# Kernel tuning notes

Hardware: AMD Instinct MI355X
Metric: run time of the kernel (lower is better)

The kernel has to match this reference:

```python
import jax, jax.numpy as jnp
import numpy as np

HEADS = 16
D_MODEL = 1024
GROUP = 4
SEQ = 2048
HEAD_DIM = D_MODEL // HEADS          # 64
KV_HEADS = HEADS // GROUP            # 4


def rope_tables(head_dim, seq_len, base=10000.0):
    # NOTE: faithful to source: exp = -2*arange(0,d,2)/d  (steps of 2 -> base^{-4j/d})
    exp = -2.0 * jnp.arange(0, head_dim, 2, dtype=jnp.float32) / head_dim
    thetas = jnp.power(base, exp)                       # [d/2]
    m = jnp.arange(seq_len, dtype=jnp.float32)          # [S]
    freq = jnp.outer(m, thetas)                         # [S, d/2]
    return jnp.cos(freq), jnp.sin(freq)


def apply_rope(x, cos, sin):
    # x: [B,S,H,D]; complex rotation on consecutive pairs
    B, S, H, D = x.shape
    xr = x.reshape(B, S, H, D // 2, 2)
    x0, x1 = xr[..., 0], xr[..., 1]
    c = cos[None, :S, None, :]
    s = sin[None, :S, None, :]
    out = jnp.stack([x0 * c - x1 * s, x0 * s + x1 * c], axis=-1)
    return out.reshape(B, S, H, D)


def setup_inputs() -> dict:
    key = jax.random.key(0)
    ks = jax.random.split(key, 8)
    B = 1
    q = jax.random.normal(ks[0], (B, SEQ, D_MODEL), dtype=jnp.float32)
    k = jax.random.normal(ks[1], (B, SEQ, D_MODEL), dtype=jnp.float32)
    v = jax.random.normal(ks[2], (B, SEQ, D_MODEL), dtype=jnp.float32)
    mask = jnp.tril(jnp.ones((SEQ, SEQ), dtype=jnp.int32))[None]  # causal [B,S,S]
    sc = 0.02
    Wq = jax.random.normal(ks[3], (D_MODEL, D_MODEL), dtype=jnp.float32) * sc
    Wk = jax.random.normal(ks[4], (D_MODEL, D_MODEL // GROUP), dtype=jnp.float32) * sc
    Wv = jax.random.normal(ks[5], (D_MODEL, D_MODEL // GROUP), dtype=jnp.float32) * sc
    Wo = jax.random.normal(ks[6], (D_MODEL, D_MODEL), dtype=jnp.float32) * sc
    bq = jnp.zeros((D_MODEL,), jnp.float32)
    bk = jnp.zeros((D_MODEL // GROUP,), jnp.float32)
    bv = jnp.zeros((D_MODEL // GROUP,), jnp.float32)
    bo = jnp.zeros((D_MODEL,), jnp.float32)
    return {"q": q, "k": k, "v": v, "mask": mask, "Wq": Wq, "bq": bq,
            "Wk": Wk, "bk": bk, "Wv": Wv, "bv": bv, "Wo": Wo, "bo": bo}


def reference(q, k, v, mask, Wq, bq, Wk, bk, Wv, bv, Wo, bo):
    B, S, _ = q.shape
    cos, sin = rope_tables(HEAD_DIM, S)
    qh = (q @ Wq + bq).reshape(B, S, HEADS, HEAD_DIM)
    kh = (k @ Wk + bk).reshape(B, S, KV_HEADS, HEAD_DIM)
    vh = (v @ Wv + bv).reshape(B, S, KV_HEADS, HEAD_DIM)
    qh = apply_rope(qh, cos, sin)
    kh = apply_rope(kh, cos, sin)
    qh = qh.transpose(0, 2, 1, 3)                       # [B,H,S,D]
    kh = kh.transpose(0, 2, 1, 3)                       # [B,Hkv,S,D]
    vh = vh.transpose(0, 2, 1, 3)
    # torch .repeat tiles: query head j attends kv head j % KV_HEADS
    kh = jnp.tile(kh, (1, GROUP, 1, 1))                 # [B,H,S,D]
    vh = jnp.tile(vh, (1, GROUP, 1, 1))
    scores = jnp.einsum('bhqd,bhkd->bhqk', qh, kh) / jnp.sqrt(
        jnp.asarray(HEAD_DIM, dtype=qh.dtype))
    scores = jnp.where(mask[:, None, :, :] == 0, -jnp.inf, scores)
    attn = jax.nn.softmax(scores, axis=-1)
    out = jnp.einsum('bhqk,bhkd->bhqd', attn, vh)
    out = out.transpose(0, 2, 1, 3).reshape(B, S, D_MODEL)
    return out @ Wo + bo
```

## Files before the change

### kernel.cpp

```cpp
#include <hip/hip_runtime.h>
#include <hip/hip_bf16.h>
#include <math.h>


#define SEQ 2048
#define DM 1024
#define HD 64

using u16 = unsigned short;
typedef __attribute__((ext_vector_type(8))) short bf16x8;
typedef __attribute__((ext_vector_type(4))) float f32x4;

#define QSCALE 0.18033688011112042f

__device__ __forceinline__ u16 f2b(float f) {
    union { float f; unsigned int i; } v; v.f = f;
    unsigned int u = v.i;
    return (u16)((u + 0x7fffu + ((u >> 16) & 1u)) >> 16);
}
__device__ __forceinline__ u16 f2b_fast(float f) {
    union { float f; unsigned int i; } v; v.f = f;
    return (u16)((v.i + 0x8000u) >> 16);
}

__global__ __launch_bounds__(256) void prep_kernel(
    const float* __restrict__ qin, const float* __restrict__ kin, const float* __restrict__ vin,
    const float* __restrict__ Wq, const float* __restrict__ Wk,
    const float* __restrict__ Wv, const float* __restrict__ Wo,
    u16* __restrict__ Xq, u16* __restrict__ Xk, u16* __restrict__ Xv,
    u16* __restrict__ Wt, u16* __restrict__ wot, float2* __restrict__ rope)
{
    const int b = blockIdx.x;
    const int t = threadIdx.x;

    if (b < 640) {
        __shared__ short T[64][72];
        const float* W; u16* dst; int N, t0, rowoff;
        if (b < 256)      { W = Wq; dst = Wt;  N = 1024; t0 = b;       rowoff = 0; }
        else if (b < 320) { W = Wk; dst = Wt;  N = 256;  t0 = b - 256; rowoff = 1024; }
        else if (b < 384) { W = Wv; dst = Wt;  N = 256;  t0 = b - 320; rowoff = 1280; }
        else              { W = Wo; dst = wot; N = 1024; t0 = b - 384; rowoff = 0; }
        const int ntn = N >> 6;
        const int k0 = (t0 / ntn) * 64, n0 = (t0 % ntn) * 64;
        const int r = t >> 4, c4 = (t & 15) * 4;
        #pragma unroll
        for (int rr = 0; rr < 4; ++rr) {
            const int k = r + rr * 16;
            float4 w4 = *reinterpret_cast<const float4*>(W + (size_t)(k0 + k) * N + n0 + c4);
            T[c4 + 0][k] = (short)f2b(w4.x);
            T[c4 + 1][k] = (short)f2b(w4.y);
            T[c4 + 2][k] = (short)f2b(w4.z);
            T[c4 + 3][k] = (short)f2b(w4.w);
        }
        __syncthreads();
        const int n = t >> 2, ck = (t & 3) * 16;
        if (b < 384) {
            const int nt = (rowoff + n0) >> 6, kt = k0 >> 6;
            char* dp = (char*)(dst + (size_t)(nt * 16 + kt) * 4096) + n * 128;
            const int g0 = (t & 3) * 2, rx = n & 7;
            *reinterpret_cast<bf16x8*>(dp + (((g0    ) ^ rx) << 4)) =
                *reinterpret_cast<const bf16x8*>(&T[n][ck]);
            *reinterpret_cast<bf16x8*>(dp + (((g0 + 1) ^ rx) << 4)) =
                *reinterpret_cast<const bf16x8*>(&T[n][ck + 8]);
        } else {
            u16* dp = dst + (size_t)(n0 + n) * DM + k0 + ck;
            *reinterpret_cast<bf16x8*>(dp)     = *reinterpret_cast<const bf16x8*>(&T[n][ck]);
            *reinterpret_cast<bf16x8*>(dp + 8) = *reinterpret_cast<const bf16x8*>(&T[n][ck + 8]);
        }
    } else if (b < 1408) {
        const int idx = b - 640;
        const int which = idx >> 8;
        const int ib = idx & 255;
        const float* src = (which == 0) ? qin : (which == 1) ? kin : vin;
        u16* dst = (which == 0) ? Xq : (which == 1) ? Xk : Xv;
        const int m  = ib * 8 + (t >> 5);
        const int mt = m >> 6, r = m & 63, rx = r & 7;
        const int col0 = (t & 31) * 32;
        const float* sp = src + (size_t)m * 1024 + col0;
        #pragma unroll
        for (int c = 0; c < 4; ++c) {
            float4 x0 = *reinterpret_cast<const float4*>(sp + c * 8);
            float4 x1 = *reinterpret_cast<const float4*>(sp + c * 8 + 4);
            bf16x8 o;
            o[0] = (short)f2b(x0.x); o[1] = (short)f2b(x0.y);
            o[2] = (short)f2b(x0.z); o[3] = (short)f2b(x0.w);
            o[4] = (short)f2b(x1.x); o[5] = (short)f2b(x1.y);
            o[6] = (short)f2b(x1.z); o[7] = (short)f2b(x1.w);
            const int col = col0 + c * 8;
            const int kt = col >> 6, g = (col & 63) >> 3;
            char* dp = (char*)(dst + (size_t)(mt * 16 + kt) * 4096)
                     + r * 128 + ((g ^ rx) << 4);
            *reinterpret_cast<bf16x8*>(dp) = o;
        }
    } else {
        const int m = (b - 1408) * 256 + t;
        float2* rp = rope + (size_t)m * 32;
        for (int pi = 0; pi < 32; ++pi) {
            const float theta = exp2f(-0.8304820237f * (float)pi);
            float sn, cs;
            sincosf((float)m * theta, &sn, &cs);
            rp[pi] = make_float2(cs, sn);
        }
    }
}

__global__ __launch_bounds__(256) void proj_mfma(
    const u16* __restrict__ Xq, const u16* __restrict__ Xk, const u16* __restrict__ Xv,
    const u16* __restrict__ Wt,
    const float* __restrict__ bq, const float* __restrict__ bk, const float* __restrict__ bv,
    const float2* __restrict__ rope,
    u16* __restrict__ Qr, u16* __restrict__ Kr, u16* __restrict__ Vrt)
{
    const int n0 = blockIdx.x * 64, m0 = blockIdx.y * 64;
    const int zone = (n0 < 1024) ? 0 : (n0 < 1280) ? 1 : 2;
    const u16* __restrict__ Az = (zone == 0) ? Xq : (zone == 1) ? Xk : Xv;

    __shared__ __align__(16) u16 As[2][4096];
    __shared__ __align__(16) u16 Bs[2][4096];

    const int t = threadIdx.x;
    const int w = t >> 6, lane = t & 63, lm = lane & 15, quad = lane >> 4;

    f32x4 acc[4] = { {0,0,0,0}, {0,0,0,0}, {0,0,0,0}, {0,0,0,0} };

    const char* Ag = (const char*)(Az + (size_t)(m0 >> 6) * 16 * 4096);
    const char* Bg = (const char*)(Wt + (size_t)(n0 >> 6) * 16 * 4096);

    auto stage = [&](int bufi, int kti) {
        const char* gA = Ag + (size_t)kti * 8192 + w * 2048 + lane * 16;
        const char* gB = Bg + (size_t)kti * 8192 + w * 2048 + lane * 16;
        char* lA = (char*)&As[bufi][0] + w * 2048;
        char* lB = (char*)&Bs[bufi][0] + w * 2048;
        #pragma unroll
        for (int i = 0; i < 2; ++i) {
            __builtin_amdgcn_global_load_lds(
                (const __attribute__((address_space(1))) unsigned int*)(gA + i * 1024),
                (__attribute__((address_space(3))) unsigned int*)(lA + i * 1024), 16, 0, 0);
            __builtin_amdgcn_global_load_lds(
                (const __attribute__((address_space(1))) unsigned int*)(gB + i * 1024),
                (__attribute__((address_space(3))) unsigned int*)(lB + i * 1024), 16, 0, 0);
        }
    };

    stage(0, 0);
    __syncthreads();

    const int rA = 16 * w + lm;
    const int axr = rA & 7;
    for (int kt = 0; kt < 16; ++kt) {
        const int buf = kt & 1;
        if (kt < 15) stage(buf ^ 1, kt + 1);
        const char* Ab = (const char*)&As[buf][0];
        const char* Bb = (const char*)&Bs[buf][0];
        bf16x8 af0 = *reinterpret_cast<const bf16x8*>(Ab + rA * 128 + (((quad    ) ^ axr) << 4));
        bf16x8 af1 = *reinterpret_cast<const bf16x8*>(Ab + rA * 128 + (((4 | quad) ^ axr) << 4));
        #pragma unroll
        for (int nb = 0; nb < 4; ++nb) {
            const int rB = 16 * nb + lm, bxr = rB & 7;
            bf16x8 b0 = *reinterpret_cast<const bf16x8*>(Bb + rB * 128 + (((quad    ) ^ bxr) << 4));
            bf16x8 b1 = *reinterpret_cast<const bf16x8*>(Bb + rB * 128 + (((4 | quad) ^ bxr) << 4));
            acc[nb] = __builtin_amdgcn_mfma_f32_16x16x32_bf16(af0, b0, acc[nb], 0, 0, 0);
            acc[nb] = __builtin_amdgcn_mfma_f32_16x16x32_bf16(af1, b1, acc[nb], 0, 0, 0);
        }
        __syncthreads();
    }

    const float* __restrict__ bias = (zone == 0) ? bq : (zone == 1) ? bk : bv;
    const int nbase = (zone == 0) ? n0 : (zone == 1) ? (n0 - 1024) : (n0 - 1280);
    const int head = nbase >> 6;
    #pragma unroll
    for (int nb = 0; nb < 4; ++nb) {
        const int d = 16 * nb + lm;
        const float bvv = bias[nbase + d];
        float vals[4];
        #pragma unroll
        for (int r = 0; r < 4; ++r) vals[r] = acc[nb][r] + bvv;
        if (zone != 2) {
            const int pi = d >> 1;
            const bool odd = (lm & 1);
            const float sca = (zone == 0) ? QSCALE : 1.0f;
            u16* op = (zone == 0 ? Qr : Kr) + (size_t)head * SEQ * HD;
            #pragma unroll
            for (int r = 0; r < 4; ++r) {
                const int m = m0 + 16 * w + quad * 4 + r;
                const float2 cs2 = rope[(size_t)m * 32 + pi];
                float x  = vals[r];
                float xp = __shfl_xor(x, 1);
                float o  = (odd ? (xp * cs2.y + x * cs2.x)
                                : (x * cs2.x - xp * cs2.y)) * sca;
                op[(size_t)m * HD + d] = f2b(o);
            }
        } else {
            u16* vp = Vrt + ((size_t)head * HD + d) * SEQ;
            #pragma unroll
            for (int r = 0; r < 4; ++r) {
                const int m = m0 + 16 * w + quad * 4 + r;
                const int within = m & 63;
                const int pos = (m & ~63) + 4 * (within & 15) + (within >> 4);
                vp[pos] = f2b(vals[r]);
            }
        }
    }
}

__global__ __launch_bounds__(256) void attn_mfma(
    const u16* __restrict__ Qr, const u16* __restrict__ Kr, const u16* __restrict__ Vrt,
    u16* __restrict__ AO)
{
    const int bid = blockIdx.x;
    const int h  = bid & 15;
    const int qt = (bid < 256) ? (bid >> 4) : 31 - ((bid - 256) >> 4);
    const int kvh = h & 3;

    __shared__ u16 Ks[2][64][72];
    __shared__ u16 Vt[2][64][72];
    __shared__ u16 Ps[4][16][76];

    const int t = threadIdx.x;
    const int w = t >> 6, lane = t & 63, lm = lane & 15, quad = lane >> 4;

    {
        const int row = lane >> 2, c = (lane & 3) * 16;
        const u16* qp = Qr + ((size_t)h * SEQ + qt * 64 + w * 16 + row) * HD + c;
        *reinterpret_cast<bf16x8*>(&Ps[w][row][c])     = *reinterpret_cast<const bf16x8*>(qp);
        *reinterpret_cast<bf16x8*>(&Ps[w][row][c + 8]) = *reinterpret_cast<const bf16x8*>(qp + 8);
    }
    const bf16x8 aq0 = *reinterpret_cast<const bf16x8*>(&Ps[w][lm][quad * 8]);
    const bf16x8 aq1 = *reinterpret_cast<const bf16x8*>(&Ps[w][lm][32 + quad * 8]);

    f32x4 O[4] = { {0,0,0,0}, {0,0,0,0}, {0,0,0,0}, {0,0,0,0} };
    float lp[4] = { 0.f, 0.f, 0.f, 0.f };

    const int srow = t >> 2, sc2 = (t & 3) * 16;
    const u16* kb_ = Kr  + ((size_t)kvh * SEQ + srow) * HD + sc2;
    const u16* vb_ = Vrt + ((size_t)kvh * HD + srow) * SEQ + sc2;
    bf16x8 kR0 = *reinterpret_cast<const bf16x8*>(kb_);
    bf16x8 kR1 = *reinterpret_cast<const bf16x8*>(kb_ + 8);
    bf16x8 vR0 = *reinterpret_cast<const bf16x8*>(vb_);
    bf16x8 vR1 = *reinterpret_cast<const bf16x8*>(vb_ + 8);

    for (int kt = 0; kt <= qt; ++kt) {
        const int buf = kt & 1;
        *reinterpret_cast<bf16x8*>(&Ks[buf][srow][sc2])     = kR0;
        *reinterpret_cast<bf16x8*>(&Ks[buf][srow][sc2 + 8]) = kR1;
        *reinterpret_cast<bf16x8*>(&Vt[buf][srow][sc2])     = vR0;
        *reinterpret_cast<bf16x8*>(&Vt[buf][srow][sc2 + 8]) = vR1;
        if (kt < qt) {
            kR0 = *reinterpret_cast<const bf16x8*>(kb_ + (size_t)(kt + 1) * 64 * HD);
            kR1 = *reinterpret_cast<const bf16x8*>(kb_ + (size_t)(kt + 1) * 64 * HD + 8);
            vR0 = *reinterpret_cast<const bf16x8*>(vb_ + (size_t)(kt + 1) * 64);
            vR1 = *reinterpret_cast<const bf16x8*>(vb_ + (size_t)(kt + 1) * 64 + 8);
        }
        __syncthreads();

        f32x4 s[4];
        #pragma unroll
        for (int nb = 0; nb < 4; ++nb) {
            bf16x8 b0 = *reinterpret_cast<const bf16x8*>(&Ks[buf][16 * nb + lm][quad * 8]);
            bf16x8 b1 = *reinterpret_cast<const bf16x8*>(&Ks[buf][16 * nb + lm][32 + quad * 8]);
            f32x4 zz = { 0.f, 0.f, 0.f, 0.f };
            zz = __builtin_amdgcn_mfma_f32_16x16x32_bf16(aq0, b0, zz, 0, 0, 0);
            s[nb] = __builtin_amdgcn_mfma_f32_16x16x32_bf16(aq1, b1, zz, 0, 0, 0);
        }

        if (kt == qt) {
            #pragma unroll
            for (int nb = 0; nb < 4; ++nb)
                #pragma unroll
                for (int r = 0; r < 4; ++r)
                    if (16 * nb + lm > 16 * w + quad * 4 + r) s[nb][r] = -INFINITY;
        }

        #pragma unroll
        for (int r = 0; r < 4; ++r) {
            u16 pk[4];
            #pragma unroll
            for (int nb = 0; nb < 4; ++nb) {
                float e = __builtin_amdgcn_exp2f(fminf(s[nb][r], 126.f));
                lp[r] += e;
                pk[nb] = f2b_fast(e);
            }
            *reinterpret_cast<uint2*>(&Ps[w][quad * 4 + r][4 * lm]) =
                *reinterpret_cast<uint2*>(pk);
        }

        const bf16x8 ap0 = *reinterpret_cast<const bf16x8*>(&Ps[w][lm][quad * 8]);
        const bf16x8 ap1 = *reinterpret_cast<const bf16x8*>(&Ps[w][lm][32 + quad * 8]);
        #pragma unroll
        for (int db = 0; db < 4; ++db) {
            bf16x8 v0 = *reinterpret_cast<const bf16x8*>(&Vt[buf][16 * db + lm][quad * 8]);
            bf16x8 v1 = *reinterpret_cast<const bf16x8*>(&Vt[buf][16 * db + lm][32 + quad * 8]);
            O[db] = __builtin_amdgcn_mfma_f32_16x16x32_bf16(ap0, v0, O[db], 0, 0, 0);
            O[db] = __builtin_amdgcn_mfma_f32_16x16x32_bf16(ap1, v1, O[db], 0, 0, 0);
        }
    }

    #pragma unroll
    for (int r = 0; r < 4; ++r) {
        #pragma unroll
        for (int off = 1; off < 16; off <<= 1)
            lp[r] += __shfl_xor(lp[r], off);
        const float inv = 1.0f / lp[r];
        const size_t row = (size_t)(qt * 64 + 16 * w + quad * 4 + r) * DM + (size_t)h * HD;
        #pragma unroll
        for (int db = 0; db < 4; ++db)
            AO[row + 16 * db + lm] = f2b(O[db][r] * inv);
    }
}

__global__ __launch_bounds__(256) void oproj_mfma(
    const u16* __restrict__ AO, const u16* __restrict__ wot,
    const float* __restrict__ bo, float* __restrict__ out)
{
    __shared__ short As[2][64][72];
    __shared__ short Bs[2][64][72];
    const int t = threadIdx.x;
    const int w = t >> 6, lane = t & 63, lm = lane & 15, quad = lane >> 4;
    const int m0 = blockIdx.y * 64, n0 = blockIdx.x * 64;
    const int sr = t >> 2, sc = (t & 3) * 16;

    f32x4 acc[4] = { {0,0,0,0}, {0,0,0,0}, {0,0,0,0}, {0,0,0,0} };

    const u16* ap_ = AO  + (size_t)(m0 + sr) * DM + sc;
    const u16* bp_ = wot + (size_t)(n0 + sr) * DM + sc;
    bf16x8 aR0 = *reinterpret_cast<const bf16x8*>(ap_);
    bf16x8 aR1 = *reinterpret_cast<const bf16x8*>(ap_ + 8);
    bf16x8 bR0 = *reinterpret_cast<const bf16x8*>(bp_);
    bf16x8 bR1 = *reinterpret_cast<const bf16x8*>(bp_ + 8);

    for (int k0 = 0; k0 < DM; k0 += 64) {
        const int buf = (k0 >> 6) & 1;
        *reinterpret_cast<bf16x8*>(&As[buf][sr][sc])     = aR0;
        *reinterpret_cast<bf16x8*>(&As[buf][sr][sc + 8]) = aR1;
        *reinterpret_cast<bf16x8*>(&Bs[buf][sr][sc])     = bR0;
        *reinterpret_cast<bf16x8*>(&Bs[buf][sr][sc + 8]) = bR1;
        if (k0 + 64 < DM) {
            aR0 = *reinterpret_cast<const bf16x8*>(ap_ + k0 + 64);
            aR1 = *reinterpret_cast<const bf16x8*>(ap_ + k0 + 72);
            bR0 = *reinterpret_cast<const bf16x8*>(bp_ + k0 + 64);
            bR1 = *reinterpret_cast<const bf16x8*>(bp_ + k0 + 72);
        }
        __syncthreads();
        bf16x8 af0 = *reinterpret_cast<const bf16x8*>(&As[buf][16 * w + lm][quad * 8]);
        bf16x8 af1 = *reinterpret_cast<const bf16x8*>(&As[buf][16 * w + lm][32 + quad * 8]);
        #pragma unroll
        for (int nb = 0; nb < 4; ++nb) {
            bf16x8 b0 = *reinterpret_cast<const bf16x8*>(&Bs[buf][16 * nb + lm][quad * 8]);
            bf16x8 b1 = *reinterpret_cast<const bf16x8*>(&Bs[buf][16 * nb + lm][32 + quad * 8]);
            acc[nb] = __builtin_amdgcn_mfma_f32_16x16x32_bf16(af0, b0, acc[nb], 0, 0, 0);
            acc[nb] = __builtin_amdgcn_mfma_f32_16x16x32_bf16(af1, b1, acc[nb], 0, 0, 0);
        }
        __syncthreads();
    }

    #pragma unroll
    for (int nb = 0; nb < 4; ++nb) {
        const int dl = 16 * nb + lm;
        const float bv = bo[n0 + dl];
        #pragma unroll
        for (int r = 0; r < 4; ++r) {
            const int m = m0 + 16 * w + quad * 4 + r;
            out[(size_t)m * DM + n0 + dl] = acc[nb][r] + bv;
        }
    }
}

extern "C" void kernel_launch(void* const* d_in, const int* in_sizes, int n_in,
                              void* d_out, int out_size, void* d_ws, size_t ws_size,
                              hipStream_t stream)
{
    const float* q  = (const float*)d_in[0];
    const float* k  = (const float*)d_in[1];
    const float* v  = (const float*)d_in[2];
    const float* Wq = (const float*)d_in[4];
    const float* bq = (const float*)d_in[5];
    const float* Wk = (const float*)d_in[6];
    const float* bk = (const float*)d_in[7];
    const float* Wv = (const float*)d_in[8];
    const float* bv = (const float*)d_in[9];
    const float* Wo = (const float*)d_in[10];
    const float* bo = (const float*)d_in[11];
    float* out = (float*)d_out;

    u16* Xq  = (u16*)d_ws;
    u16* Xk  = Xq  + (size_t)SEQ * DM;
    u16* Xv  = Xk  + (size_t)SEQ * DM;
    u16* Wt  = Xv  + (size_t)SEQ * DM;
    u16* wot = Wt  + (size_t)1536 * 1024;
    u16* Qr  = wot + (size_t)1024 * 1024;
    u16* Kr  = Qr  + (size_t)16 * SEQ * HD;
    u16* Vrt = Kr  + (size_t)4 * SEQ * HD;
    u16* AO  = Vrt + (size_t)4 * SEQ * HD;
    float2* rope = (float2*)(AO + (size_t)SEQ * DM);

    hipLaunchKernelGGL(prep_kernel, dim3(1416), dim3(256), 0, stream,
                       q, k, v, Wq, Wk, Wv, Wo, Xq, Xk, Xv, Wt, wot, rope);
    hipLaunchKernelGGL(proj_mfma, dim3(24, 32), dim3(256), 0, stream,
                       Xq, Xk, Xv, Wt, bq, bk, bv, rope, Qr, Kr, Vrt);
    hipLaunchKernelGGL(attn_mfma, dim3(512), dim3(256), 0, stream,
                       Qr, Kr, Vrt, AO);
    hipLaunchKernelGGL(oproj_mfma, dim3(16, 32), dim3(256), 0, stream,
                       AO, wot, bo, out);
}
```

Baseline: 165.4 us.

## Halve attention query tile to 32 rows with XOR-swizzled unpadded LDS

The attention kernel now uses 128-thread blocks covering 32 query rows each, launched as 1024 blocks. This doubles the grid for better CU fill and causal load balance, but each K/V tile is now loaded by twice as many blocks. K/V shared tiles drop their padding and use an XOR swizzle on 16-byte chunks to avoid bank conflicts. The bf16 conversion of softmax probabilities now uses the packed v_cvt_pk_bf16_f32 instruction instead of manual bit rounding.

```diff
diff --git a/kernel.cpp b/kernel.cpp
--- a/kernel.cpp
+++ b/kernel.cpp
@@ -18,9 +18,10 @@
     unsigned int u = v.i;
     return (u16)((u + 0x7fffu + ((u >> 16) & 1u)) >> 16);
 }
-__device__ __forceinline__ u16 f2b_fast(float f) {
-    union { float f; unsigned int i; } v; v.f = f;
-    return (u16)((v.i + 0x8000u) >> 16);
+__device__ __forceinline__ unsigned int cvtpk(float lo, float hi) {
+    unsigned int r;
+    asm("v_cvt_pk_bf16_f32 %0, %1, %2" : "=v"(r) : "v"(lo), "v"(hi));
+    return r;
 }
 
 __global__ __launch_bounds__(256) void prep_kernel(
@@ -203,25 +204,25 @@
     }
 }
 
-__global__ __launch_bounds__(256) void attn_mfma(
+__global__ __launch_bounds__(128) void attn_mfma(
     const u16* __restrict__ Qr, const u16* __restrict__ Kr, const u16* __restrict__ Vrt,
     u16* __restrict__ AO)
 {
     const int bid = blockIdx.x;
     const int h  = bid & 15;
-    const int qt = (bid < 256) ? (bid >> 4) : 31 - ((bid - 256) >> 4);
+    const int qt = (bid < 512) ? (bid >> 4) : 63 - ((bid - 512) >> 4);
     const int kvh = h & 3;
 
-    __shared__ u16 Ks[2][64][72];
-    __shared__ u16 Vt[2][64][72];
-    __shared__ u16 Ps[4][16][76];
+    __shared__ __align__(16) u16 Ks[2][64][64];
+    __shared__ __align__(16) u16 Vt[2][64][64];
+    __shared__ u16 Ps[2][16][76];
 
     const int t = threadIdx.x;
     const int w = t >> 6, lane = t & 63, lm = lane & 15, quad = lane >> 4;
 
     {
         const int row = lane >> 2, c = (lane & 3) * 16;
-        const u16* qp = Qr + ((size_t)h * SEQ + qt * 64 + w * 16 + row) * HD + c;
+        const u16* qp = Qr + ((size_t)h * SEQ + qt * 32 + w * 16 + row) * HD + c;
         *reinterpret_cast<bf16x8*>(&Ps[w][row][c])     = *reinterpret_cast<const bf16x8*>(qp);
         *reinterpret_cast<bf16x8*>(&Ps[w][row][c + 8]) = *reinterpret_cast<const bf16x8*>(qp + 8);
     }
@@ -231,65 +232,78 @@
     f32x4 O[4] = { {0,0,0,0}, {0,0,0,0}, {0,0,0,0}, {0,0,0,0} };
     float lp[4] = { 0.f, 0.f, 0.f, 0.f };
 
-    const int srow = t >> 2, sc2 = (t & 3) * 16;
-    const u16* kb_ = Kr  + ((size_t)kvh * SEQ + srow) * HD + sc2;
-    const u16* vb_ = Vrt + ((size_t)kvh * HD + srow) * SEQ + sc2;
-    bf16x8 kR0 = *reinterpret_cast<const bf16x8*>(kb_);
-    bf16x8 kR1 = *reinterpret_cast<const bf16x8*>(kb_ + 8);
-    bf16x8 vR0 = *reinterpret_cast<const bf16x8*>(vb_);
-    bf16x8 vR1 = *reinterpret_cast<const bf16x8*>(vb_ + 8);
-
-    for (int kt = 0; kt <= qt; ++kt) {
+    const int srow = t >> 1, half = t & 1, sxr = srow & 7;
+    const u16* kb_ = Kr  + ((size_t)kvh * SEQ + srow) * HD + half * 32;
+    const u16* vb_ = Vrt + ((size_t)kvh * HD + srow) * SEQ + half * 32;
+    bf16x8 kR[4], vR[4];
+    #pragma unroll
+    for (int i = 0; i < 4; ++i) {
+        kR[i] = *reinterpret_cast<const bf16x8*>(kb_ + 8 * i);
+        vR[i] = *reinterpret_cast<const bf16x8*>(vb_ + 8 * i);
+    }
+
+    const int KT = qt >> 1;
+    const int radd = 32 * (qt & 1);
+    for (int kt = 0; kt <= KT; ++kt) {
         const int buf = kt & 1;
-        *reinterpret_cast<bf16x8*>(&Ks[buf][srow][sc2])     = kR0;
-        *reinterpret_cast<bf16x8*>(&Ks[buf][srow][sc2 + 8]) = kR1;
-        *reinterpret_cast<bf16x8*>(&Vt[buf][srow][sc2])     = vR0;
-        *reinterpret_cast<bf16x8*>(&Vt[buf][srow][sc2 + 8]) = vR1;
-        if (kt < qt) {
-            kR0 = *reinterpret_cast<const bf16x8*>(kb_ + (size_t)(kt + 1) * 64 * HD);
-            kR1 = *reinterpret_cast<const bf16x8*>(kb_ + (size_t)(kt + 1) * 64 * HD + 8);
-            vR0 = *reinterpret_cast<const bf16x8*>(vb_ + (size_t)(kt + 1) * 64);
-            vR1 = *reinterpret_cast<const bf16x8*>(vb_ + (size_t)(kt + 1) * 64 + 8);
+        {
+            char* kdst = (char*)&Ks[buf][0][0] + srow * 128;
+            char* vdst = (char*)&Vt[buf][0][0] + srow * 128;
+            #pragma unroll
+            for (int i = 0; i < 4; ++i) {
+                *reinterpret_cast<bf16x8*>(kdst + (((4 * half + i) ^ sxr) << 4)) = kR[i];
+                *reinterpret_cast<bf16x8*>(vdst + (((4 * half + i) ^ sxr) << 4)) = vR[i];
+            }
+        }
+        if (kt < KT) {
+            #pragma unroll
+            for (int i = 0; i < 4; ++i) {
+                kR[i] = *reinterpret_cast<const bf16x8*>(kb_ + (size_t)(kt + 1) * 64 * HD + 8 * i);
+                vR[i] = *reinterpret_cast<const bf16x8*>(vb_ + (size_t)(kt + 1) * 64 + 8 * i);
+            }
         }
         __syncthreads();
 
+        const int xr = lm & 7;
         f32x4 s[4];
         #pragma unroll
         for (int nb = 0; nb < 4; ++nb) {
-            bf16x8 b0 = *reinterpret_cast<const bf16x8*>(&Ks[buf][16 * nb + lm][quad * 8]);
-            bf16x8 b1 = *reinterpret_cast<const bf16x8*>(&Ks[buf][16 * nb + lm][32 + quad * 8]);
+            const char* kb = (const char*)&Ks[buf][0][0] + (16 * nb + lm) * 128;
+            bf16x8 b0 = *reinterpret_cast<const bf16x8*>(kb + (((quad    ) ^ xr) << 4));
+            bf16x8 b1 = *reinterpret_cast<const bf16x8*>(kb + (((4 | quad) ^ xr) << 4));
             f32x4 zz = { 0.f, 0.f, 0.f, 0.f };
             zz = __builtin_amdgcn_mfma_f32_16x16x32_bf16(aq0, b0, zz, 0, 0, 0);
             s[nb] = __builtin_amdgcn_mfma_f32_16x16x32_bf16(aq1, b1, zz, 0, 0, 0);
         }
 
-        if (kt == qt) {
+        if (kt == KT) {
             #pragma unroll
             for (int nb = 0; nb < 4; ++nb)
                 #pragma unroll
                 for (int r = 0; r < 4; ++r)
-                    if (16 * nb + lm > 16 * w + quad * 4 + r) s[nb][r] = -INFINITY;
+                    if (16 * nb + lm > 16 * w + quad * 4 + r + radd) s[nb][r] = -INFINITY;
         }
 
         #pragma unroll
         for (int r = 0; r < 4; ++r) {
-            u16 pk[4];
-            #pragma unroll
-            for (int nb = 0; nb < 4; ++nb) {
-                float e = __builtin_amdgcn_exp2f(fminf(s[nb][r], 126.f));
-                lp[r] += e;
-                pk[nb] = f2b_fast(e);
-            }
-            *reinterpret_cast<uint2*>(&Ps[w][quad * 4 + r][4 * lm]) =
-                *reinterpret_cast<uint2*>(pk);
+            float e0 = __builtin_amdgcn_exp2f(fminf(s[0][r], 126.f));
+            float e1 = __builtin_amdgcn_exp2f(fminf(s[1][r], 126.f));
+            float e2 = __builtin_amdgcn_exp2f(fminf(s[2][r], 126.f));
+            float e3 = __builtin_amdgcn_exp2f(fminf(s[3][r], 126.f));
+            lp[r] += (e0 + e1) + (e2 + e3);
+            uint2 pk2;
+            pk2.x = cvtpk(e0, e1);
+            pk2.y = cvtpk(e2, e3);
+            *reinterpret_cast<uint2*>(&Ps[w][quad * 4 + r][4 * lm]) = pk2;
         }
 
         const bf16x8 ap0 = *reinterpret_cast<const bf16x8*>(&Ps[w][lm][quad * 8]);
         const bf16x8 ap1 = *reinterpret_cast<const bf16x8*>(&Ps[w][lm][32 + quad * 8]);
         #pragma unroll
         for (int db = 0; db < 4; ++db) {
-            bf16x8 v0 = *reinterpret_cast<const bf16x8*>(&Vt[buf][16 * db + lm][quad * 8]);
-            bf16x8 v1 = *reinterpret_cast<const bf16x8*>(&Vt[buf][16 * db + lm][32 + quad * 8]);
+            const char* vb = (const char*)&Vt[buf][0][0] + (16 * db + lm) * 128;
+            bf16x8 v0 = *reinterpret_cast<const bf16x8*>(vb + (((quad    ) ^ xr) << 4));
+            bf16x8 v1 = *reinterpret_cast<const bf16x8*>(vb + (((4 | quad) ^ xr) << 4));
             O[db] = __builtin_amdgcn_mfma_f32_16x16x32_bf16(ap0, v0, O[db], 0, 0, 0);
             O[db] = __builtin_amdgcn_mfma_f32_16x16x32_bf16(ap1, v1, O[db], 0, 0, 0);
         }
@@ -301,7 +315,7 @@
         for (int off = 1; off < 16; off <<= 1)
             lp[r] += __shfl_xor(lp[r], off);
         const float inv = 1.0f / lp[r];
-        const size_t row = (size_t)(qt * 64 + 16 * w + quad * 4 + r) * DM + (size_t)h * HD;
+        const size_t row = (size_t)(qt * 32 + 16 * w + quad * 4 + r) * DM + (size_t)h * HD;
         #pragma unroll
         for (int db = 0; db < 4; ++db)
             AO[row + 16 * db + lm] = f2b(O[db][r] * inv);
@@ -397,7 +411,7 @@
                        q, k, v, Wq, Wk, Wv, Wo, Xq, Xk, Xv, Wt, wot, rope);
     hipLaunchKernelGGL(proj_mfma, dim3(24, 32), dim3(256), 0, stream,
                        Xq, Xk, Xv, Wt, bq, bk, bv, rope, Qr, Kr, Vrt);
-    hipLaunchKernelGGL(attn_mfma, dim3(512), dim3(256), 0, stream,
+    hipLaunchKernelGGL(attn_mfma, dim3(1024), dim3(128), 0, stream,
                        Qr, Kr, Vrt, AO);
     hipLaunchKernelGGL(oproj_mfma, dim3(16, 32), dim3(256), 0, stream,
                        AO, wot, bo, out);
```

Measured after the change: 169.2 us. 2.3% more time.
